# Performance work log

Hardware: AMD Instinct MI355X
Metric: run time of the kernel (lower is better)

The kernel has to match this reference:

```python
import jax, jax.numpy as jnp
import numpy as np

B = 2048   # windows per stream
N = 49     # tokens per 7x7 window
C = 192    # dim
H = 6      # heads
D = C // H # head_dim = 32
WH = WW = 7
SCALE = D ** -0.5


def _rel_pos_index():
    coords = np.stack(np.meshgrid(np.arange(WH), np.arange(WW), indexing='ij')).reshape(2, -1)
    rc = (coords[:, :, None] - coords[:, None, :]).transpose(1, 2, 0)  # [N,N,2]
    rc[..., 0] += WH - 1
    rc[..., 1] += WW - 1
    rc[..., 0] *= 2 * WW - 1
    return rc.sum(-1)  # [N,N] ints in [0, 169)

RPI = _rel_pos_index()


def setup_inputs() -> dict:
    key = jax.random.key(0)
    ks = jax.random.split(key, 16)
    w = lambda k, sh: jax.random.normal(k, sh, jnp.float32) * 0.02
    s = lambda v: jnp.asarray(v, jnp.float32)
    return {
        'x_sa': jax.random.normal(ks[0], (2 * B, N, C), jnp.float32),
        'x_ca': jax.random.normal(ks[1], (B, 2 * N, C), jnp.float32),
        'lambda_sa': s(0.1),
        'lambda_ca': s(0.1),
        'sa_enh': s(0.1),
        'ca_enh': s(0.1),
        'W_sa_qkv': w(ks[2], (C, 3 * C)), 'b_sa_qkv': jnp.zeros((3 * C,), jnp.float32),
        'W_sa_ct': w(ks[3], (C, C)), 'W_sa_cr': w(ks[4], (C, C)),
        'W_ca_q': w(ks[5], (C, C)), 'b_ca_q': jnp.zeros((C,), jnp.float32),
        'W_ca_kv': w(ks[6], (C, 2 * C)), 'b_ca_kv': jnp.zeros((2 * C,), jnp.float32),
        'W_ca_ct': w(ks[7], (C, C)), 'W_ca_cr': w(ks[8], (C, C)),
        'rpb_table': w(ks[9], ((2 * WH - 1) * (2 * WW - 1), H)),
        'W_proj_sa': w(ks[10], (C, C)), 'b_proj_sa': jnp.zeros((C,), jnp.float32),
        'W_proj_ca': w(ks[11], (C, C)), 'b_proj_ca': jnp.zeros((C,), jnp.float32),
    }


def _heads(x):  # [B,N,C] -> [B,H,N,D]
    b, n, _ = x.shape
    return x.reshape(b, n, H, D).transpose(0, 2, 1, 3)


def _merge(x):  # [B,H,N,D] -> [B,N,C]
    b = x.shape[0]
    return x.transpose(0, 2, 1, 3).reshape(b, -1, C)


def _diff_attn(qt, kt, vt, qr, kr, vr, bias, lam_param):
    at = jax.nn.softmax(jnp.einsum('bhnd,bhmd->bhnm', qt * SCALE, kt) + bias, axis=-1)
    ar = jax.nn.softmax(jnp.einsum('bhnd,bhmd->bhnm', qr * SCALE, kr) + bias, axis=-1)
    lam = jnp.clip(jax.nn.sigmoid(lam_param), 0.01, 0.99)
    ot = jnp.einsum('bhnm,bhmd->bhnd', at - lam * ar, vt)
    orf = jnp.einsum('bhnm,bhmd->bhnd', ar - lam * at, vr)
    return ot, orf


def _forward(x_sa, x_ca, lambda_sa, lambda_ca, sa_enh, ca_enh,
             W_sa_qkv, b_sa_qkv, W_sa_ct, W_sa_cr,
             W_ca_q, b_ca_q, W_ca_kv, b_ca_kv, W_ca_ct, W_ca_cr,
             rpb_table, W_proj_sa, b_proj_sa, W_proj_ca, b_proj_ca):
    bias = rpb_table[RPI.reshape(-1)].reshape(N, N, H).transpose(2, 0, 1)  # [H,N,N]

    # ---- self-attention path (streams concat on batch) ----
    xt, xr = x_sa[:B], x_sa[B:]
    te = xt + sa_enh * (xr @ W_sa_cr)
    re = xr + sa_enh * (xt @ W_sa_ct)
    qkv_t = (te @ W_sa_qkv + b_sa_qkv).reshape(B, N, 3, H, D).transpose(2, 0, 3, 1, 4)
    qkv_r = (re @ W_sa_qkv + b_sa_qkv).reshape(B, N, 3, H, D).transpose(2, 0, 3, 1, 4)
    ot, orf = _diff_attn(qkv_t[0], qkv_t[1], qkv_t[2], qkv_r[0], qkv_r[1], qkv_r[2], bias, lambda_sa)
    out_sa = jnp.concatenate([_merge(ot) @ W_proj_sa + b_proj_sa,
                              _merge(orf) @ W_proj_sa + b_proj_sa], axis=0)  # [2B,N,C]

    # ---- cross-attention path (streams concat on sequence) ----
    xt, xr = x_ca[:, :N, :], x_ca[:, N:, :]
    te = xt + ca_enh * (xr @ W_ca_cr)
    re = xr + ca_enh * (xt @ W_ca_ct)
    qt = _heads(te @ W_ca_q + b_ca_q)
    qr = _heads(re @ W_ca_q + b_ca_q)
    xcat = jnp.concatenate([te, re], axis=1)  # [B,2N,C]
    kv = (xcat @ W_ca_kv + b_ca_kv).reshape(B, 2 * N, 2, H, D).transpose(2, 0, 3, 1, 4)
    k, v = kv[0], kv[1]  # [B,H,2N,D]
    ot, orf = _diff_attn(qt, k[:, :, :N], v[:, :, :N], qr, k[:, :, N:], v[:, :, N:], bias, lambda_ca)
    out_ca = jnp.concatenate([_merge(ot) @ W_proj_ca + b_proj_ca,
                              _merge(orf) @ W_proj_ca + b_proj_ca], axis=1)  # [B,2N,C]

    return jnp.stack([out_sa, out_ca.reshape(2 * B, N, C)], axis=0)  # [2,2B,N,C]


def reference(x_sa, x_ca, lambda_sa, lambda_ca, sa_enh, ca_enh,
              W_sa_qkv, b_sa_qkv, W_sa_ct, W_sa_cr,
              W_ca_q, b_ca_q, W_ca_kv, b_ca_kv, W_ca_ct, W_ca_cr,
              rpb_table, W_proj_sa, b_proj_sa, W_proj_ca, b_proj_ca):
    return _forward(x_sa, x_ca, lambda_sa, lambda_ca, sa_enh, ca_enh,
                    W_sa_qkv, b_sa_qkv, W_sa_ct, W_sa_cr,
                    W_ca_q, b_ca_q, W_ca_kv, b_ca_kv, W_ca_ct, W_ca_cr,
                    rpb_table, W_proj_sa, b_proj_sa, W_proj_ca, b_proj_ca)
```

## Files before the change

### kernel.cpp

```cpp
#include <hip/hip_runtime.h>
#include <cmath>

static constexpr float SCALE_ = 0.17677669529663687f;

typedef __attribute__((ext_vector_type(8))) _Float16 f16x8;
typedef __attribute__((ext_vector_type(8))) ushort u16x8;
typedef __attribute__((ext_vector_type(4))) float f32x4;

__device__ inline ushort f16u(float f) {
    union { _Float16 h; ushort u; } c;
    c.h = (_Float16)f;
    return c.u;
}

__device__ __forceinline__ void gld16(const ushort* g, ushort* l) {
    __builtin_amdgcn_global_load_lds(
        (const __attribute__((address_space(1))) unsigned int*)g,
        (__attribute__((address_space(3))) unsigned int*)l,
        16, 0, 0);
}

__global__ __launch_bounds__(256) void smallmm_kernel(
    const float* __restrict__ Wa, const float* __restrict__ Wb,
    const float* __restrict__ scale_p, float* __restrict__ out, int NCb)
{
    int idx = blockIdx.x * 256 + threadIdx.x;
    int n4  = NCb >> 2;
    int m   = idx / n4;
    int n0  = (idx - m * n4) << 2;
    if (m >= 192) return;
    float s = scale_p[0];
    float ax = 0.f, ay = 0.f, az = 0.f, aw = 0.f;
    for (int k = 0; k < 192; ++k) {
        float a = Wa[m * 192 + k];
        const float4 b = *(const float4*)(Wb + (size_t)k * NCb + n0);
        ax += a * b.x; ay += a * b.y; az += a * b.z; aw += a * b.w;
    }
    float4 r = make_float4(ax * s, ay * s, az * s, aw * s);
    *(float4*)(out + (size_t)m * NCb + n0) = r;
}

__global__ __launch_bounds__(256) void conv_x(
    const float* __restrict__ src, long long src_bs,
    ushort* __restrict__ dh, int Mc)
{
    const long long SS = (long long)Mc * 32;
    const long long total8 = (long long)Mc * 24;
    for (long long t = (long long)blockIdx.x * 256 + threadIdx.x; t < total8;
         t += (long long)gridDim.x * 256) {
        int m  = (int)(t / 24);
        int c8 = (int)(t - (long long)m * 24) * 8;
        int bb = m / 49, r = m - bb * 49;
        const float* sp = src + (long long)bb * src_bs + r * 192 + c8;
        float4 v0 = *(const float4*)sp;
        float4 v1 = *(const float4*)(sp + 4);
        float f[8] = {v0.x, v0.y, v0.z, v0.w, v1.x, v1.y, v1.z, v1.w};
        u16x8 h8;
        #pragma unroll
        for (int e = 0; e < 8; ++e) h8[e] = f16u(f[e]);
        long long o = (long long)(c8 >> 5) * SS + (long long)m * 32 + (c8 & 31);
        *(u16x8*)(dh + o) = h8;
    }
}

__global__ __launch_bounds__(256) void conv_wT(
    const float* __restrict__ W, int NC, ushort* __restrict__ dh)
{
    int idx = blockIdx.x * 256 + threadIdx.x;
    if (idx >= NC * 192) return;
    int n = idx / 192, k = idx - n * 192;
    float f = W[(long long)k * NC + n];
    long long o = ((long long)(k >> 5) * NC + n) * 32 + (k & 31);
    dh[o] = f16u(f);
}

template<int NC, bool DUAL, bool F32OUT>
__global__ __launch_bounds__(256, 4) void gemm_f16(
    const ushort* __restrict__ Ah1, const ushort* __restrict__ Ah2,
    const ushort* __restrict__ Bh1, const ushort* __restrict__ Bh2,
    const float* __restrict__ bias,
    ushort* __restrict__ outH,
    float* __restrict__ outF, long long out_bs,
    int M)
{
    __shared__ __align__(16) ushort AHs[2048];
    __shared__ __align__(16) ushort BHs[6144];

    const int tid = threadIdx.x;
    const int lane = tid & 63, wv = tid >> 6;
    const int wm = (wv >> 1) * 32;
    const int wn = (wv & 1) * 96;
    const int lr = lane & 15, lg = lane >> 4;
    const int bn = blockIdx.x, bm = blockIdx.y;
    const long long SS = (long long)M * 32;
    constexpr int NS = DUAL ? 12 : 6;

    const int at_row = tid >> 2;
    const int at_c   = (tid & 3) ^ ((tid >> 3) & 3);
    const long long a_src = (long long)(bm * 64 + at_row) * 32 + at_c * 8;
    int b_src[3];
    #pragma unroll
    for (int k = 0; k < 3; ++k) {
        int t = k * 256 + tid;
        int row = t >> 2, c = (t & 3) ^ ((t >> 3) & 3);
        b_src[k] = (bn * 192 + row) * 32 + c * 8;
    }
    const int wdst = wv * 512;

    int aoff[2], boff[6];
    #pragma unroll
    for (int i = 0; i < 2; ++i) {
        int row = wm + 16 * i + lr;
        aoff[i] = (row * 4 + (lg ^ ((row >> 1) & 3))) * 8;
    }
    #pragma unroll
    for (int j = 0; j < 6; ++j) {
        int row = wn + 16 * j + lr;
        boff[j] = (row * 4 + (lg ^ ((row >> 1) & 3))) * 8;
    }

    f32x4 acc[2][6] = {};

    #pragma unroll
    for (int s = 0; s < NS; ++s) {
        const int k6 = (s < 6) ? s : s - 6;
        const ushort* AHp = (!DUAL || s < 6) ? Ah1 : Ah2;
        const ushort* BHp = (!DUAL || s < 6) ? Bh1 : Bh2;
        const long long asb = (long long)k6 * SS;
        const int bsb = k6 * (NC * 32);

        gld16(AHp + asb + a_src, AHs + wdst);
        #pragma unroll
        for (int k = 0; k < 3; ++k)
            gld16(BHp + bsb + b_src[k], BHs + k * 2048 + wdst);
        __syncthreads();

        f16x8 ah[2];
        #pragma unroll
        for (int i = 0; i < 2; ++i)
            ah[i] = *(const f16x8*)&AHs[aoff[i]];
        #pragma unroll
        for (int j = 0; j < 6; ++j) {
            f16x8 bh = *(const f16x8*)&BHs[boff[j]];
            #pragma unroll
            for (int i = 0; i < 2; ++i)
                acc[i][j] = __builtin_amdgcn_mfma_f32_16x16x32_f16(ah[i], bh, acc[i][j], 0, 0, 0);
        }
        __syncthreads();
    }

    #pragma unroll
    for (int j = 0; j < 6; ++j) {
        const int c = bn * 192 + wn + 16 * j + lr;
        const float bv = bias ? bias[c] : 0.f;
        #pragma unroll
        for (int i = 0; i < 2; ++i)
            #pragma unroll
            for (int r = 0; r < 4; ++r) {
                int m = bm * 64 + wm + 16 * i + 4 * lg + r;
                if (m < M) {
                    float f = acc[i][j][r] + bv;
                    if constexpr (F32OUT) {
                        int b2 = m / 49, r2 = m - b2 * 49;
                        outF[(long long)b2 * out_bs + r2 * 192 + c] = f;
                    } else {
                        long long o = (long long)(c >> 5) * SS + (long long)m * 32 + (c & 31);
                        outH[o] = f16u(f);
                    }
                }
            }
    }
}

__global__ __launch_bounds__(256, 4) void attn_f16(
    const ushort* __restrict__ qT, const ushort* __restrict__ kT,
    const ushort* __restrict__ vT,
    const ushort* __restrict__ qR, const ushort* __restrict__ kR,
    const ushort* __restrict__ vR,
    long long SS,
    const float* __restrict__ rpb, const float* __restrict__ lam_ptr,
    ushort* __restrict__ otH, ushort* __restrict__ orH)
{
    __shared__ __align__(16) ushort Pth[64][72];
    __shared__ __align__(16) ushort Vs[2][32][70];
    __shared__ float bias_s[169];

    const int tid = threadIdx.x;
    const int bb = blockIdx.x / 6;
    const int h  = blockIdx.x - bb * 6;
    const int lane = tid & 63;
    const int w  = tid >> 6;
    const int li = lane & 15;
    const int lg = lane >> 4;
    const long long rowbase = (long long)bb * 49 * 32;
    const long long hb = (long long)h * SS + rowbase;

    for (int idx = tid; idx < 169; idx += 256) bias_s[idx] = rpb[idx * 6 + h];

    {
        const ushort* vsrc[2] = {vT + hb, vR + hb};
        for (int c = tid; c < 392; c += 256) {
            int s  = c / 196;
            int r2 = c - s * 196;
            int j  = r2 >> 2;
            int d4 = (r2 & 3) * 8;
            u16x8 v = *(const u16x8*)(vsrc[s] + j * 32 + d4);
            #pragma unroll
            for (int e = 0; e < 8; ++e) Vs[s][d4 + e][j] = v[e];
        }
        for (int c = tid; c < 2 * 32 * 21; c += 256) {
            int s  = c / (32 * 21);
            int r1 = c - s * (32 * 21);
            int d  = r1 / 21;
            int j  = 49 + (r1 - d * 21);
            Vs[s][d][j] = 0;
        }
    }

    float lraw = lam_ptr[0];
    float lam = 1.f / (1.f + __expf(-lraw));
    lam = fminf(fmaxf(lam, 0.01f), 0.99f);

    const int irow = min(w * 16 + li, 48);

    f32x4 st[2][4];
    #pragma unroll
    for (int s = 0; s < 2; ++s) {
        const ushort* qb = (s ? qR : qT) + hb;
        const ushort* kb = (s ? kR : kT) + hb;
        f16x8 qh = *(const f16x8*)(qb + irow * 32 + 8 * lg);
        #pragma unroll
        for (int jt = 0; jt < 4; ++jt) {
            int jr = jt * 16 + li; if (jr > 48) jr = 48;
            f16x8 kh = *(const f16x8*)(kb + jr * 32 + 8 * lg);
            f32x4 c = {};
            c = __builtin_amdgcn_mfma_f32_16x16x32_f16(kh, qh, c, 0, 0, 0);
            st[s][jt] = c;
        }
    }
    __syncthreads();

    const int ri = (irow * 9363) >> 16;
    const int ci = irow - 7 * ri;
    float bias_v[4][4];
    #pragma unroll
    for (int jt = 0; jt < 4; ++jt)
        #pragma unroll
        for (int r = 0; r < 4; ++r) {
            int j = jt * 16 + 4 * lg + r;
            int jc = (j < 49) ? j : 48;
            int rj = (jc * 9363) >> 16;
            int cj = jc - 7 * rj;
            bias_v[jt][r] = bias_s[(ri - rj + 6) * 13 + (ci - cj + 6)];
        }

    float p[2][4][4];
    #pragma unroll
    for (int s = 0; s < 2; ++s) {
        float m = -1e30f;
        #pragma unroll
        for (int jt = 0; jt < 4; ++jt)
            #pragma unroll
            for (int r = 0; r < 4; ++r) {
                int j = jt * 16 + 4 * lg + r;
                float sv = (j < 49) ? (st[s][jt][r] * SCALE_ + bias_v[jt][r]) : -1e30f;
                p[s][jt][r] = sv;
                m = fmaxf(m, sv);
            }
        m = fmaxf(m, __shfl_xor(m, 16));
        m = fmaxf(m, __shfl_xor(m, 32));
        float sum = 0.f;
        #pragma unroll
        for (int jt = 0; jt < 4; ++jt)
            #pragma unroll
            for (int r = 0; r < 4; ++r) {
                float e = __expf(p[s][jt][r] - m);
                p[s][jt][r] = e;
                sum += e;
            }
        sum += __shfl_xor(sum, 16);
        sum += __shfl_xor(sum, 32);
        float inv = 1.f / sum;
        #pragma unroll
        for (int jt = 0; jt < 4; ++jt)
            #pragma unroll
            for (int r = 0; r < 4; ++r)
                p[s][jt][r] *= inv;
    }

    const int prow = w * 16 + li;
    #pragma unroll
    for (int s = 0; s < 2; ++s) {
        #pragma unroll
        for (int jt = 0; jt < 4; ++jt) {
            ushort4 h4;
            #pragma unroll
            for (int r = 0; r < 4; ++r) {
                float at = p[0][jt][r], ar = p[1][jt][r];
                float f = (s == 0) ? (at - lam * ar) : (ar - lam * at);
                ((ushort*)&h4)[r] = f16u(f);
            }
            *(ushort4*)&Pth[prow][jt * 16 + 4 * lg] = h4;
        }

        f32x4 acc[2] = {};
        #pragma unroll
        for (int ks = 0; ks < 2; ++ks) {
            f16x8 pa = *(const f16x8*)&Pth[prow][ks * 32 + 8 * lg];
            #pragma unroll
            for (int dt = 0; dt < 2; ++dt) {
                f16x8 vh = *(const f16x8*)&Vs[s][dt * 16 + li][ks * 32 + 8 * lg];
                acc[dt] = __builtin_amdgcn_mfma_f32_16x16x32_f16(pa, vh, acc[dt], 0, 0, 0);
            }
        }
        ushort* oph = s ? orH : otH;
        #pragma unroll
        for (int dt = 0; dt < 2; ++dt)
            #pragma unroll
            for (int r = 0; r < 4; ++r) {
                int i = w * 16 + 4 * lg + r;
                if (i < 49) {
                    long long o = (long long)h * SS + rowbase + (long long)i * 32 + dt * 16 + li;
                    oph[o] = f16u(acc[dt][r]);
                }
            }
    }
}

extern "C" void kernel_launch(void* const* d_in, const int* in_sizes, int n_in,
                              void* d_out, int out_size, void* d_ws, size_t ws_size,
                              hipStream_t stream)
{
    const float* x_sa      = (const float*)d_in[0];
    const float* x_ca      = (const float*)d_in[1];
    const float* lam_sa    = (const float*)d_in[2];
    const float* lam_ca    = (const float*)d_in[3];
    const float* sa_enh    = (const float*)d_in[4];
    const float* ca_enh    = (const float*)d_in[5];
    const float* W_sa_qkv  = (const float*)d_in[6];
    const float* b_sa_qkv  = (const float*)d_in[7];
    const float* W_sa_ct   = (const float*)d_in[8];
    const float* W_sa_cr   = (const float*)d_in[9];
    const float* W_ca_q    = (const float*)d_in[10];
    const float* b_ca_q    = (const float*)d_in[11];
    const float* W_ca_kv   = (const float*)d_in[12];
    const float* b_ca_kv   = (const float*)d_in[13];
    const float* W_ca_ct   = (const float*)d_in[14];
    const float* W_ca_cr   = (const float*)d_in[15];
    const float* rpb       = (const float*)d_in[16];
    const float* W_proj_sa = (const float*)d_in[17];
    const float* b_proj_sa = (const float*)d_in[18];
    const float* W_proj_ca = (const float*)d_in[19];
    const float* b_proj_ca = (const float*)d_in[20];
    float* out = (float*)d_out;
    float* ws  = (float*)d_ws;

    float* CW0 = ws;
    float* CW1 = CW0 + 110592;
    float* CW2 = CW1 + 110592;
    float* CW3 = CW2 + 36864;
    float* CW4 = CW3 + 36864;
    float* CW5 = CW4 + 73728;

    smallmm_kernel<<<108, 256, 0, stream>>>(W_sa_cr, W_sa_qkv, sa_enh, CW0, 576);
    smallmm_kernel<<<108, 256, 0, stream>>>(W_sa_ct, W_sa_qkv, sa_enh, CW1, 576);
    smallmm_kernel<<< 36, 256, 0, stream>>>(W_ca_cr, W_ca_q,   ca_enh, CW2, 192);
    smallmm_kernel<<< 36, 256, 0, stream>>>(W_ca_ct, W_ca_q,   ca_enh, CW3, 192);
    smallmm_kernel<<< 72, 256, 0, stream>>>(W_ca_cr, W_ca_kv,  ca_enh, CW4, 384);
    smallmm_kernel<<< 72, 256, 0, stream>>>(W_ca_ct, W_ca_kv,  ca_enh, CW5, 384);

    ushort* wb = (ushort*)(ws + 442368);
    ushort* WsaqH = wb;
    ushort* C0H  = WsaqH + 110592;
    ushort* C1H  = C0H + 110592;
    ushort* WcqH = C1H + 110592;
    ushort* C2H  = WcqH + 36864;
    ushort* C3H  = C2H + 36864;
    ushort* WckH = C3H + 36864;
    ushort* C4H  = WckH + 73728;
    ushort* C5H  = C4H + 73728;
    ushort* WpsH = C5H + 73728;
    ushort* WpcH = WpsH + 36864;
    ushort* chunkU = WpcH + 36864;

    conv_wT<<<432, 256, 0, stream>>>(W_sa_qkv, 576, WsaqH);
    conv_wT<<<432, 256, 0, stream>>>(CW0,      576, C0H);
    conv_wT<<<432, 256, 0, stream>>>(CW1,      576, C1H);
    conv_wT<<<144, 256, 0, stream>>>(W_ca_q,   192, WcqH);
    conv_wT<<<144, 256, 0, stream>>>(CW2,      192, C2H);
    conv_wT<<<144, 256, 0, stream>>>(CW3,      192, C3H);
    conv_wT<<<288, 256, 0, stream>>>(W_ca_kv,  384, WckH);
    conv_wT<<<288, 256, 0, stream>>>(CW4,      384, C4H);
    conv_wT<<<288, 256, 0, stream>>>(CW5,      384, C5H);
    conv_wT<<<144, 256, 0, stream>>>(W_proj_sa,192, WpsH);
    conv_wT<<<144, 256, 0, stream>>>(W_proj_ca,192, WpcH);

    long long avail = (long long)ws_size - 442368LL * 4 - 737280LL * 2 - 65536;
    int cbmax = (int)(avail / 188160);
    if (cbmax > 2048) cbmax = 2048;
    if (cbmax < 1) cbmax = 1;

    const long long OUT1 = 2LL * 2048 * 49 * 192;
    dim3 blk(256);

    for (int c0 = 0; c0 < 2048; c0 += cbmax) {
        int cb = (c0 + cbmax <= 2048) ? cbmax : (2048 - c0);
        int M = cb * 49;
        long long SS = (long long)M * 32;
        int gy = (M + 63) / 64;
        int cblk = (int)(((long long)M * 24 + 255) / 256);
        if (cblk > 4096) cblk = 4096;

        dim3 g1(3, gy), g2(1, gy), g3(2, gy);

        ushort* XtH = chunkU;
        ushort* XrH = XtH + (long long)cbmax * 9408;
        ushort* QtH = XrH + (long long)cbmax * 9408;
        ushort* QrH = QtH + (long long)cbmax * 28224;
        ushort* OtH = QrH + (long long)cbmax * 28224;
        ushort* OrH = OtH + (long long)cbmax * 9408;

        conv_x<<<cblk, blk, 0, stream>>>(x_sa + (long long)c0 * 9408, 9408, XtH, M);
        conv_x<<<cblk, blk, 0, stream>>>(x_sa + (2048LL + c0) * 9408, 9408, XrH, M);

        gemm_f16<576, true, false><<<g1, blk, 0, stream>>>(
            XtH, XrH, WsaqH, C0H, b_sa_qkv, QtH, nullptr, 0, M);
        gemm_f16<576, true, false><<<g1, blk, 0, stream>>>(
            XrH, XtH, WsaqH, C1H, b_sa_qkv, QrH, nullptr, 0, M);

        attn_f16<<<cb * 6, blk, 0, stream>>>(
            QtH, QtH + 6 * SS, QtH + 12 * SS,
            QrH, QrH + 6 * SS, QrH + 12 * SS,
            SS, rpb, lam_sa, OtH, OrH);

        gemm_f16<192, false, true><<<g2, blk, 0, stream>>>(
            OtH, nullptr, WpsH, nullptr, b_proj_sa, nullptr,
            out + (long long)c0 * 9408, 9408, M);
        gemm_f16<192, false, true><<<g2, blk, 0, stream>>>(
            OrH, nullptr, WpsH, nullptr, b_proj_sa, nullptr,
            out + (2048LL + c0) * 9408, 9408, M);

        ushort* CXtH = chunkU;
        ushort* CXrH = CXtH + (long long)cbmax * 9408;
        ushort* CQtH = CXrH + (long long)cbmax * 9408;
        ushort* CQrH = CQtH + (long long)cbmax * 9408;
        ushort* KtH  = CQrH + (long long)cbmax * 9408;
        ushort* KrH  = KtH + (long long)cbmax * 18816;
        ushort* COtH = KrH + (long long)cbmax * 18816;
        ushort* COrH = COtH + (long long)cbmax * 9408;

        conv_x<<<cblk, blk, 0, stream>>>(x_ca + (long long)c0 * 18816, 18816, CXtH, M);
        conv_x<<<cblk, blk, 0, stream>>>(x_ca + (long long)c0 * 18816 + 9408, 18816, CXrH, M);

        gemm_f16<192, true, false><<<g2, blk, 0, stream>>>(
            CXtH, CXrH, WcqH, C2H, b_ca_q, CQtH, nullptr, 0, M);
        gemm_f16<192, true, false><<<g2, blk, 0, stream>>>(
            CXrH, CXtH, WcqH, C3H, b_ca_q, CQrH, nullptr, 0, M);

        gemm_f16<384, true, false><<<g3, blk, 0, stream>>>(
            CXtH, CXrH, WckH, C4H, b_ca_kv, KtH, nullptr, 0, M);
        gemm_f16<384, true, false><<<g3, blk, 0, stream>>>(
            CXrH, CXtH, WckH, C5H, b_ca_kv, KrH, nullptr, 0, M);

        attn_f16<<<cb * 6, blk, 0, stream>>>(
            CQtH, KtH, KtH + 6 * SS,
            CQrH, KrH, KrH + 6 * SS,
            SS, rpb, lam_ca, COtH, COrH);

        gemm_f16<192, false, true><<<g2, blk, 0, stream>>>(
            COtH, nullptr, WpcH, nullptr, b_proj_ca, nullptr,
            out + OUT1 + (long long)c0 * 18816, 18816, M);
        gemm_f16<192, false, true><<<g2, blk, 0, stream>>>(
            COrH, nullptr, WpcH, nullptr, b_proj_ca, nullptr,
            out + OUT1 + (long long)c0 * 18816 + 9408, 18816, M);
    }
}
```

Measured before the change: 898.2 us.

## Batch kernel launches and load two K-steps per barrier in GEMM

The six small weight-product launches become one job-table kernel, and the eleven weight-transpose launches become another. Paired input conversions and paired GEMMs are merged into single launches, using blockIdx.z to select the stream. Inside the GEMM, two K-slices are loaded into doubled LDS buffers before each barrier, which halves the barrier count. This cuts launch count and sync overhead, but the doubled LDS (about 32 KB per block) may lower occupancy below the requested 4 blocks per CU.

```diff
diff --git a/kernel.cpp b/kernel.cpp
--- a/kernel.cpp
+++ b/kernel.cpp
@@ -20,36 +20,75 @@
         16, 0, 0);
 }
 
-__global__ __launch_bounds__(256) void smallmm_kernel(
-    const float* __restrict__ Wa, const float* __restrict__ Wb,
-    const float* __restrict__ scale_p, float* __restrict__ out, int NCb)
+struct SmallmmJobs {
+    const float* Wa[6];
+    const float* Wb[6];
+    const float* sc[6];
+    float*       out[6];
+    int          NCb[6];
+    int          base[7];
+};
+__global__ __launch_bounds__(256) void smallmm_all(SmallmmJobs J)
 {
-    int idx = blockIdx.x * 256 + threadIdx.x;
+    int b = blockIdx.x;
+    int j = 0;
+    #pragma unroll
+    for (int k = 1; k < 6; ++k) if (b >= J.base[k]) j = k;
+    int idx = (b - J.base[j]) * 256 + threadIdx.x;
+    int NCb = J.NCb[j];
     int n4  = NCb >> 2;
     int m   = idx / n4;
     int n0  = (idx - m * n4) << 2;
     if (m >= 192) return;
-    float s = scale_p[0];
+    const float* Wa = J.Wa[j];
+    const float* Wb = J.Wb[j];
+    float s = J.sc[j][0];
     float ax = 0.f, ay = 0.f, az = 0.f, aw = 0.f;
     for (int k = 0; k < 192; ++k) {
         float a = Wa[m * 192 + k];
-        const float4 b = *(const float4*)(Wb + (size_t)k * NCb + n0);
-        ax += a * b.x; ay += a * b.y; az += a * b.z; aw += a * b.w;
+        const float4 bv = *(const float4*)(Wb + (size_t)k * NCb + n0);
+        ax += a * bv.x; ay += a * bv.y; az += a * bv.z; aw += a * bv.w;
     }
     float4 r = make_float4(ax * s, ay * s, az * s, aw * s);
-    *(float4*)(out + (size_t)m * NCb + n0) = r;
-}
-
-__global__ __launch_bounds__(256) void conv_x(
-    const float* __restrict__ src, long long src_bs,
-    ushort* __restrict__ dh, int Mc)
+    *(float4*)(J.out[j] + (size_t)m * NCb + n0) = r;
+}
+
+struct WtJobs {
+    const float* W[11];
+    ushort*      dh[11];
+    int          NC[11];
+    int          base[12];
+};
+__global__ __launch_bounds__(256) void conv_wT_all(WtJobs J)
+{
+    int b = blockIdx.x;
+    int j = 0;
+    #pragma unroll
+    for (int k = 1; k < 11; ++k) if (b >= J.base[k]) j = k;
+    int idx = (b - J.base[j]) * 256 + threadIdx.x;
+    int NC = J.NC[j];
+    if (idx >= NC * 192) return;
+    int n = idx / 192, k = idx - n * 192;
+    float f = J.W[j][(long long)k * NC + n];
+    long long o = ((long long)(k >> 5) * NC + n) * 32 + (k & 31);
+    J.dh[j][o] = f16u(f);
+}
+
+__global__ __launch_bounds__(256) void conv_x2(
+    const float* __restrict__ src_t, const float* __restrict__ src_r,
+    long long src_bs,
+    ushort* __restrict__ dh_t, ushort* __restrict__ dh_r, int Mc)
 {
     const long long SS = (long long)Mc * 32;
     const long long total8 = (long long)Mc * 24;
-    for (long long t = (long long)blockIdx.x * 256 + threadIdx.x; t < total8;
+    for (long long t = (long long)blockIdx.x * 256 + threadIdx.x; t < 2 * total8;
          t += (long long)gridDim.x * 256) {
-        int m  = (int)(t / 24);
-        int c8 = (int)(t - (long long)m * 24) * 8;
+        const int second = (t >= total8);
+        long long ti = second ? t - total8 : t;
+        const float* src = second ? src_r : src_t;
+        ushort* dh = second ? dh_r : dh_t;
+        int m  = (int)(ti / 24);
+        int c8 = (int)(ti - (long long)m * 24) * 8;
         int bb = m / 49, r = m - bb * 49;
         const float* sp = src + (long long)bb * src_bs + r * 192 + c8;
         float4 v0 = *(const float4*)sp;
@@ -63,28 +102,24 @@
     }
 }
 
-__global__ __launch_bounds__(256) void conv_wT(
-    const float* __restrict__ W, int NC, ushort* __restrict__ dh)
-{
-    int idx = blockIdx.x * 256 + threadIdx.x;
-    if (idx >= NC * 192) return;
-    int n = idx / 192, k = idx - n * 192;
-    float f = W[(long long)k * NC + n];
-    long long o = ((long long)(k >> 5) * NC + n) * 32 + (k & 31);
-    dh[o] = f16u(f);
-}
-
 template<int NC, bool DUAL, bool F32OUT>
 __global__ __launch_bounds__(256, 4) void gemm_f16(
-    const ushort* __restrict__ Ah1, const ushort* __restrict__ Ah2,
-    const ushort* __restrict__ Bh1, const ushort* __restrict__ Bh2,
-    const float* __restrict__ bias,
-    ushort* __restrict__ outH,
-    float* __restrict__ outF, long long out_bs,
-    int M)
+    const ushort* __restrict__ A1a, const ushort* __restrict__ A2a,
+    const ushort* __restrict__ B2a, ushort* __restrict__ outHa,
+    float* __restrict__ outFa,
+    const ushort* __restrict__ A1b, const ushort* __restrict__ A2b,
+    const ushort* __restrict__ B2b, ushort* __restrict__ outHb,
+    float* __restrict__ outFb,
+    const ushort* __restrict__ B1, const float* __restrict__ bias,
+    long long out_bs, int M)
 {
-    __shared__ __align__(16) ushort AHs[2048];
-    __shared__ __align__(16) ushort BHs[6144];
+    __shared__ __align__(16) ushort AHs[2][2048];
+    __shared__ __align__(16) ushort BHs[2][6144];
+
+    const int z = blockIdx.z;
+    const ushort* Ah1 = z ? A1b : A1a;
+    const ushort* Ah2 = z ? A2b : A2a;
+    const ushort* Bh2 = z ? B2b : B2a;
 
     const int tid = threadIdx.x;
     const int lane = tid & 63, wv = tid >> 6;
@@ -93,7 +128,7 @@
     const int lr = lane & 15, lg = lane >> 4;
     const int bn = blockIdx.x, bm = blockIdx.y;
     const long long SS = (long long)M * 32;
-    constexpr int NS = DUAL ? 12 : 6;
+    constexpr int NP = DUAL ? 6 : 3;
 
     const int at_row = tid >> 2;
     const int at_c   = (tid & 3) ^ ((tid >> 3) & 3);
@@ -122,29 +157,35 @@
     f32x4 acc[2][6] = {};
 
     #pragma unroll
-    for (int s = 0; s < NS; ++s) {
-        const int k6 = (s < 6) ? s : s - 6;
-        const ushort* AHp = (!DUAL || s < 6) ? Ah1 : Ah2;
-        const ushort* BHp = (!DUAL || s < 6) ? Bh1 : Bh2;
-        const long long asb = (long long)k6 * SS;
-        const int bsb = k6 * (NC * 32);
-
-        gld16(AHp + asb + a_src, AHs + wdst);
-        #pragma unroll
-        for (int k = 0; k < 3; ++k)
-            gld16(BHp + bsb + b_src[k], BHs + k * 2048 + wdst);
+    for (int p = 0; p < NP; ++p) {
+        #pragma unroll
+        for (int hbf = 0; hbf < 2; ++hbf) {
+            const int s = 2 * p + hbf;
+            const int k6 = (s < 6) ? s : s - 6;
+            const ushort* AHp = (!DUAL || s < 6) ? Ah1 : Ah2;
+            const ushort* BHp = (!DUAL || s < 6) ? B1  : Bh2;
+            const long long asb = (long long)k6 * SS;
+            const int bsb = k6 * (NC * 32);
+            gld16(AHp + asb + a_src, AHs[hbf] + wdst);
+            #pragma unroll
+            for (int k = 0; k < 3; ++k)
+                gld16(BHp + bsb + b_src[k], BHs[hbf] + k * 2048 + wdst);
+        }
         __syncthreads();
 
-        f16x8 ah[2];
-        #pragma unroll
-        for (int i = 0; i < 2; ++i)
-            ah[i] = *(const f16x8*)&AHs[aoff[i]];
-        #pragma unroll
-        for (int j = 0; j < 6; ++j) {
-            f16x8 bh = *(const f16x8*)&BHs[boff[j]];
+        #pragma unroll
+        for (int hbf = 0; hbf < 2; ++hbf) {
+            f16x8 ah[2];
             #pragma unroll
             for (int i = 0; i < 2; ++i)
-                acc[i][j] = __builtin_amdgcn_mfma_f32_16x16x32_f16(ah[i], bh, acc[i][j], 0, 0, 0);
+                ah[i] = *(const f16x8*)&AHs[hbf][aoff[i]];
+            #pragma unroll
+            for (int j = 0; j < 6; ++j) {
+                f16x8 bh = *(const f16x8*)&BHs[hbf][boff[j]];
+                #pragma unroll
+                for (int i = 0; i < 2; ++i)
+                    acc[i][j] = __builtin_amdgcn_mfma_f32_16x16x32_f16(ah[i], bh, acc[i][j], 0, 0, 0);
+            }
         }
         __syncthreads();
     }
@@ -161,9 +202,11 @@
                 if (m < M) {
                     float f = acc[i][j][r] + bv;
                     if constexpr (F32OUT) {
+                        float* outF = z ? outFb : outFa;
                         int b2 = m / 49, r2 = m - b2 * 49;
                         outF[(long long)b2 * out_bs + r2 * 192 + c] = f;
                     } else {
+                        ushort* outH = z ? outHb : outHa;
                         long long o = (long long)(c >> 5) * SS + (long long)m * 32 + (c & 31);
                         outH[o] = f16u(f);
                     }
@@ -362,12 +405,18 @@
     float* CW4 = CW3 + 36864;
     float* CW5 = CW4 + 73728;
 
-    smallmm_kernel<<<108, 256, 0, stream>>>(W_sa_cr, W_sa_qkv, sa_enh, CW0, 576);
-    smallmm_kernel<<<108, 256, 0, stream>>>(W_sa_ct, W_sa_qkv, sa_enh, CW1, 576);
-    smallmm_kernel<<< 36, 256, 0, stream>>>(W_ca_cr, W_ca_q,   ca_enh, CW2, 192);
-    smallmm_kernel<<< 36, 256, 0, stream>>>(W_ca_ct, W_ca_q,   ca_enh, CW3, 192);
-    smallmm_kernel<<< 72, 256, 0, stream>>>(W_ca_cr, W_ca_kv,  ca_enh, CW4, 384);
-    smallmm_kernel<<< 72, 256, 0, stream>>>(W_ca_ct, W_ca_kv,  ca_enh, CW5, 384);
+    {
+        SmallmmJobs J;
+        J.Wa[0]=W_sa_cr; J.Wb[0]=W_sa_qkv; J.sc[0]=sa_enh; J.out[0]=CW0; J.NCb[0]=576;
+        J.Wa[1]=W_sa_ct; J.Wb[1]=W_sa_qkv; J.sc[1]=sa_enh; J.out[1]=CW1; J.NCb[1]=576;
+        J.Wa[2]=W_ca_cr; J.Wb[2]=W_ca_q;   J.sc[2]=ca_enh; J.out[2]=CW2; J.NCb[2]=192;
+        J.Wa[3]=W_ca_ct; J.Wb[3]=W_ca_q;   J.sc[3]=ca_enh; J.out[3]=CW3; J.NCb[3]=192;
+        J.Wa[4]=W_ca_cr; J.Wb[4]=W_ca_kv;  J.sc[4]=ca_enh; J.out[4]=CW4; J.NCb[4]=384;
+        J.Wa[5]=W_ca_ct; J.Wb[5]=W_ca_kv;  J.sc[5]=ca_enh; J.out[5]=CW5; J.NCb[5]=384;
+        int bs[7] = {0,108,216,252,288,360,432};
+        for (int i = 0; i < 7; ++i) J.base[i] = bs[i];
+        smallmm_all<<<432, 256, 0, stream>>>(J);
+    }
 
     ushort* wb = (ushort*)(ws + 442368);
     ushort* WsaqH = wb;
@@ -383,17 +432,18 @@
     ushort* WpcH = WpsH + 36864;
     ushort* chunkU = WpcH + 36864;
 
-    conv_wT<<<432, 256, 0, stream>>>(W_sa_qkv, 576, WsaqH);
-    conv_wT<<<432, 256, 0, stream>>>(CW0,      576, C0H);
-    conv_wT<<<432, 256, 0, stream>>>(CW1,      576, C1H);
-    conv_wT<<<144, 256, 0, stream>>>(W_ca_q,   192, WcqH);
-    conv_wT<<<144, 256, 0, stream>>>(CW2,      192, C2H);
-    conv_wT<<<144, 256, 0, stream>>>(CW3,      192, C3H);
-    conv_wT<<<288, 256, 0, stream>>>(W_ca_kv,  384, WckH);
-    conv_wT<<<288, 256, 0, stream>>>(CW4,      384, C4H);
-    conv_wT<<<288, 256, 0, stream>>>(CW5,      384, C5H);
-    conv_wT<<<144, 256, 0, stream>>>(W_proj_sa,192, WpsH);
-    conv_wT<<<144, 256, 0, stream>>>(W_proj_ca,192, WpcH);
+    {
+        WtJobs J;
+        const float* Ws[11] = {W_sa_qkv, CW0, CW1, W_ca_q, CW2, CW3,
+                               W_ca_kv, CW4, CW5, W_proj_sa, W_proj_ca};
+        ushort* Ds[11] = {WsaqH, C0H, C1H, WcqH, C2H, C3H,
+                          WckH, C4H, C5H, WpsH, WpcH};
+        int NCs[11] = {576,576,576,192,192,192,384,384,384,192,192};
+        int bs[12] = {0,432,864,1296,1440,1584,1728,2016,2304,2592,2736,2880};
+        for (int i = 0; i < 11; ++i) { J.W[i]=Ws[i]; J.dh[i]=Ds[i]; J.NC[i]=NCs[i]; }
+        for (int i = 0; i < 12; ++i) J.base[i] = bs[i];
+        conv_wT_all<<<2880, 256, 0, stream>>>(J);
+    }
 
     long long avail = (long long)ws_size - 442368LL * 4 - 737280LL * 2 - 65536;
     int cbmax = (int)(avail / 188160);
@@ -408,10 +458,10 @@
         int M = cb * 49;
         long long SS = (long long)M * 32;
         int gy = (M + 63) / 64;
-        int cblk = (int)(((long long)M * 24 + 255) / 256);
+        int cblk = (int)(((long long)M * 48 + 255) / 256);
         if (cblk > 4096) cblk = 4096;
 
-        dim3 g1(3, gy), g2(1, gy), g3(2, gy);
+        dim3 g1(3, gy, 2), g2(1, gy, 2), g3(2, gy, 2);
 
         ushort* XtH = chunkU;
         ushort* XrH = XtH + (long long)cbmax * 9408;
@@ -420,13 +470,14 @@
         ushort* OtH = QrH + (long long)cbmax * 28224;
         ushort* OrH = OtH + (long long)cbmax * 9408;
 
-        conv_x<<<cblk, blk, 0, stream>>>(x_sa + (long long)c0 * 9408, 9408, XtH, M);
-        conv_x<<<cblk, blk, 0, stream>>>(x_sa + (2048LL + c0) * 9408, 9408, XrH, M);
+        conv_x2<<<cblk, blk, 0, stream>>>(
+            x_sa + (long long)c0 * 9408, x_sa + (2048LL + c0) * 9408, 9408,
+            XtH, XrH, M);
 
         gemm_f16<576, true, false><<<g1, blk, 0, stream>>>(
-            XtH, XrH, WsaqH, C0H, b_sa_qkv, QtH, nullptr, 0, M);
-        gemm_f16<576, true, false><<<g1, blk, 0, stream>>>(
-            XrH, XtH, WsaqH, C1H, b_sa_qkv, QrH, nullptr, 0, M);
+            XtH, XrH, C0H, QtH, nullptr,
+            XrH, XtH, C1H, QrH, nullptr,
+            WsaqH, b_sa_qkv, 0, M);
 
         attn_f16<<<cb * 6, blk, 0, stream>>>(
             QtH, QtH + 6 * SS, QtH + 12 * SS,
@@ -434,11 +485,9 @@
             SS, rpb, lam_sa, OtH, OrH);
 
         gemm_f16<192, false, true><<<g2, blk, 0, stream>>>(
-            OtH, nullptr, WpsH, nullptr, b_proj_sa, nullptr,
-            out + (long long)c0 * 9408, 9408, M);
-        gemm_f16<192, false, true><<<g2, blk, 0, stream>>>(
-            OrH, nullptr, WpsH, nullptr, b_proj_sa, nullptr,
-            out + (2048LL + c0) * 9408, 9408, M);
+            OtH, nullptr, nullptr, nullptr, out + (long long)c0 * 9408,
+            OrH, nullptr, nullptr, nullptr, out + (2048LL + c0) * 9408,
+            WpsH, b_proj_sa, 9408, M);
 
         ushort* CXtH = chunkU;
         ushort* CXrH = CXtH + (long long)cbmax * 9408;
@@ -449,18 +498,19 @@
         ushort* COtH = KrH + (long long)cbmax * 18816;
         ushort* COrH = COtH + (long long)cbmax * 9408;
 
-        conv_x<<<cblk, blk, 0, stream>>>(x_ca + (long long)c0 * 18816, 18816, CXtH, M);
-        conv_x<<<cblk, blk, 0, stream>>>(x_ca + (long long)c0 * 18816 + 9408, 18816, CXrH, M);
+        conv_x2<<<cblk, blk, 0, stream>>>(
+            x_ca + (long long)c0 * 18816, x_ca + (long long)c0 * 18816 + 9408, 18816,
+            CXtH, CXrH, M);
 
         gemm_f16<192, true, false><<<g2, blk, 0, stream>>>(
-            CXtH, CXrH, WcqH, C2H, b_ca_q, CQtH, nullptr, 0, M);
-        gemm_f16<192, true, false><<<g2, blk, 0, stream>>>(
-            CXrH, CXtH, WcqH, C3H, b_ca_q, CQrH, nullptr, 0, M);
+            CXtH, CXrH, C2H, CQtH, nullptr,
+            CXrH, CXtH, C3H, CQrH, nullptr,
+            WcqH, b_ca_q, 0, M);
 
         gemm_f16<384, true, false><<<g3, blk, 0, stream>>>(
-            CXtH, CXrH, WckH, C4H, b_ca_kv, KtH, nullptr, 0, M);
-        gemm_f16<384, true, false><<<g3, blk, 0, stream>>>(
-            CXrH, CXtH, WckH, C5H, b_ca_kv, KrH, nullptr, 0, M);
+            CXtH, CXrH, C4H, KtH, nullptr,
+            CXrH, CXtH, C5H, KrH, nullptr,
+            WckH, b_ca_kv, 0, M);
 
         attn_f16<<<cb * 6, blk, 0, stream>>>(
             CQtH, KtH, KtH + 6 * SS,
@@ -468,10 +518,8 @@
             SS, rpb, lam_ca, COtH, COrH);
 
         gemm_f16<192, false, true><<<g2, blk, 0, stream>>>(
-            COtH, nullptr, WpcH, nullptr, b_proj_ca, nullptr,
-            out + OUT1 + (long long)c0 * 18816, 18816, M);
-        gemm_f16<192, false, true><<<g2, blk, 0, stream>>>(
-            COrH, nullptr, WpcH, nullptr, b_proj_ca, nullptr,
-            out + OUT1 + (long long)c0 * 18816 + 9408, 18816, M);
-    }
-}
+            COtH, nullptr, nullptr, nullptr, out + OUT1 + (long long)c0 * 18816,
+            COrH, nullptr, nullptr, nullptr, out + OUT1 + (long long)c0 * 18816 + 9408,
+            WpcH, b_proj_ca, 18816, M);
+    }
+}
```

Measured after the change: 795.7 us. 1.13x faster.
